# Optimization experiments

Measured on AMD Instinct MI355X. Metric: run time of the kernel, lower is better.

The kernel has to match this reference:

```python
import jax, jax.numpy as jnp
import numpy as np

D_MODEL = 2048
N_HEADS = 16
HEAD_DIM = D_MODEL // N_HEADS  # 128
B, S = 4, 2048


def setup_inputs() -> dict:
    key = jax.random.key(0)
    ks = jax.random.split(key, 7)
    scale = 1.0 / np.sqrt(D_MODEL)
    return {
        "x": jax.random.normal(ks[0], (B, S, D_MODEL), dtype=jnp.float32),
        "cos": jax.random.uniform(ks[1], (S, HEAD_DIM // 2), dtype=jnp.float32),
        "sin": jax.random.uniform(ks[2], (S, HEAD_DIM // 2), dtype=jnp.float32),
        "Wq": jax.random.normal(ks[3], (D_MODEL, D_MODEL), dtype=jnp.float32) * scale,
        "Wk": jax.random.normal(ks[4], (D_MODEL, D_MODEL), dtype=jnp.float32) * scale,
        "Wv": jax.random.normal(ks[5], (D_MODEL, D_MODEL), dtype=jnp.float32) * scale,
        "Wo": jax.random.normal(ks[6], (D_MODEL, D_MODEL), dtype=jnp.float32) * scale,
    }


def apply_rope(x, cos, sin):
    # x: [B, H, S, head_dim]; cos/sin: [S, half] (split-in-half RoPE)
    half = x.shape[-1] // 2
    x1, x2 = x[..., :half], x[..., half:]
    cos = cos[None, None, :, :].astype(x.dtype)
    sin = sin[None, None, :, :].astype(x.dtype)
    return jnp.concatenate([x1 * cos - x2 * sin, x1 * sin + x2 * cos], axis=-1)


def reference(x, cos, sin, Wq, Wk, Wv, Wo):
    Bx, Sx, _ = x.shape
    # nn.Linear: y = x @ W.T
    def proj(W):
        y = jnp.einsum("bsd,ed->bse", x, W)
        return y.reshape(Bx, Sx, N_HEADS, HEAD_DIM).transpose(0, 2, 1, 3)  # [B,H,S,hd]
    q = apply_rope(proj(Wq), cos, sin)
    k = apply_rope(proj(Wk), cos, sin)
    v = proj(Wv)
    scale = 1.0 / np.sqrt(HEAD_DIM)
    scores = jnp.einsum("bhqd,bhkd->bhqk", q, k) * scale  # [B,H,S,S]
    attn = jax.nn.softmax(scores, axis=-1)
    out = jnp.einsum("bhqk,bhkd->bhqd", attn, v)
    out = out.transpose(0, 2, 1, 3).reshape(Bx, Sx, D_MODEL)
    return jnp.einsum("bsd,ed->bse", out, Wo)
```

## Files before the change

### kernel.cpp

```cpp
#include <hip/hip_runtime.h>

typedef _Float16 half_t;
typedef __attribute__((ext_vector_type(8))) _Float16 half8;
typedef __attribute__((ext_vector_type(4))) _Float16 half4v;
typedef __attribute__((ext_vector_type(4))) float f32x4;

#define MFMA16(a,b,c) __builtin_amdgcn_mfma_f32_16x16x32_f16((a),(b),(c),0,0,0)

__device__ __forceinline__ void gld_lds16(const half_t* g, half_t* l){
    __builtin_amdgcn_global_load_lds((__attribute__((address_space(1))) void*)(g),
                                     (__attribute__((address_space(3))) void*)(l), 16, 0, 0);
}

__global__ __launch_bounds__(256) void cvt_k(const float* __restrict__ s, half_t* __restrict__ d, int n4){
    int i = blockIdx.x * 256 + threadIdx.x;
    if (i < n4){
        float4 v = ((const float4*)s)[i];
        half4v h = { (half_t)v.x, (half_t)v.y, (half_t)v.z, (half_t)v.w };
        ((half4v*)d)[i] = h;
    }
}

__global__ __launch_bounds__(256) void cvtw_k(const float* __restrict__ w0, const float* __restrict__ w1,
                                              const float* __restrict__ w2, const float* __restrict__ w3,
                                              half_t* __restrict__ dst){
    const float* srcs[4] = {w0, w1, w2, w3};
    const float* s = srcs[blockIdx.y];
    int i = blockIdx.x * 256 + threadIdx.x;
    float4 v = ((const float4*)s)[i];
    half4v h = { (half_t)v.x, (half_t)v.y, (half_t)v.z, (half_t)v.w };
    ((half4v*)(dst))[(size_t)blockIdx.y * 1048576 + i] = h;
}

__global__ __launch_bounds__(256) void gemm_nt(const half_t* __restrict__ A, const half_t* __restrict__ B,
                                               half_t* __restrict__ Qw, half_t* __restrict__ Kw,
                                               half_t* __restrict__ Vt, float* __restrict__ Co, int kind){
    const int tid  = threadIdx.x;
    const int lane = tid & 63;
    const int w    = lane >> 4;
    const int l15  = lane & 15;
    const int l7   = lane & 7;
    const int wav  = tid >> 6;
    const int wm   = (wav >> 1) * 64;
    const int wn   = (wav & 1) * 64;
    const int bm   = blockIdx.x;
    const int bn   = blockIdx.y;
    const int KD   = 2048;

    __shared__ __align__(16) half_t smem[16384];
    half_t* As = smem;
    half_t* Bs = smem + 8192;

    f32x4 acc[4][4] = {};

    const half_t* Ab = A + (size_t)bm * 128 * KD;
    const half_t* Bb = B + (size_t)bn * 128 * KD;

    for (int k0 = 0; k0 < KD; k0 += 64){
#pragma unroll
        for (int i = 0; i < 4; i++){
            int c = tid + i*256;
            int r = c >> 3, p = c & 7;
            gld_lds16(Ab + (size_t)r*KD + k0 + ((p ^ (r&7)) << 3), As + c*8);
        }
#pragma unroll
        for (int i = 0; i < 4; i++){
            int c = tid + i*256;
            int r = c >> 3, p = c & 7;
            gld_lds16(Bb + (size_t)r*KD + k0 + ((p ^ (r&7)) << 3), Bs + c*8);
        }
        __syncthreads();
#pragma unroll
        for (int ks = 0; ks < 2; ks++){
            half8 af[4], bf[4];
#pragma unroll
            for (int mi = 0; mi < 4; mi++)
                af[mi] = *(const half8*)(As + (wm + mi*16 + l15)*64 + (((ks*4 + w) ^ l7) << 3));
#pragma unroll
            for (int ni = 0; ni < 4; ni++)
                bf[ni] = *(const half8*)(Bs + (wn + ni*16 + l15)*64 + (((ks*4 + w) ^ l7) << 3));
#pragma unroll
            for (int mi = 0; mi < 4; mi++)
#pragma unroll
                for (int ni = 0; ni < 4; ni++)
                    acc[mi][ni] = MFMA16(af[mi], bf[ni], acc[mi][ni]);
        }
        __syncthreads();
    }

    const int rbase = wm + w*4;
    const int cbase = wn + l15;

    if (kind == 0){
        const int which = bn >> 4;
        const int nb = (bn & 15) * 128;
        if (which < 2){
            half_t* dst = which ? Kw : Qw;
#pragma unroll
            for (int mi = 0; mi < 4; mi++)
#pragma unroll
                for (int ni = 0; ni < 4; ni++)
#pragma unroll
                    for (int r = 0; r < 4; r++){
                        int m = bm*128 + rbase + mi*16 + r;
                        int n = nb + cbase + ni*16;
                        dst[(((size_t)(m>>11)*16 + (n>>7))*2048 + (m&2047))*128 + (n&127)] = (half_t)acc[mi][ni][r];
                    }
        } else {
#pragma unroll
            for (int mi = 0; mi < 4; mi++)
#pragma unroll
                for (int ni = 0; ni < 4; ni++){
                    int m0 = bm*128 + rbase + mi*16;
                    int n  = nb + cbase + ni*16;
                    half4v h = {(half_t)acc[mi][ni][0], (half_t)acc[mi][ni][1],
                                (half_t)acc[mi][ni][2], (half_t)acc[mi][ni][3]};
                    *(half4v*)(Vt + (((size_t)(m0>>11)*16 + (n>>7))*128 + (n&127))*2048 + (m0&2047)) = h;
                }
        }
    } else {
#pragma unroll
        for (int mi = 0; mi < 4; mi++)
#pragma unroll
            for (int ni = 0; ni < 4; ni++)
#pragma unroll
                for (int r = 0; r < 4; r++){
                    int m = bm*128 + rbase + mi*16 + r;
                    int n = bn*128 + cbase + ni*16;
                    Co[(size_t)m*2048 + n] = acc[mi][ni][r];
                }
    }
}

__global__ __launch_bounds__(256) void rope_k(half_t* __restrict__ Qw, half_t* __restrict__ Kw,
                                              const float* __restrict__ cs, const float* __restrict__ sn){
    int t  = blockIdx.x * 256 + threadIdx.x;
    int d  = t & 63;
    int s  = (t >> 6) & 2047;
    int bh = t >> 17;
    float c  = cs[s*64 + d];
    float si = sn[s*64 + d];
    size_t base = ((size_t)bh*2048 + s)*128 + d;
    float q1 = (float)Qw[base], q2 = (float)Qw[base+64];
    Qw[base]    = (half_t)(q1*c - q2*si);
    Qw[base+64] = (half_t)(q1*si + q2*c);
    float k1 = (float)Kw[base], k2 = (float)Kw[base+64];
    Kw[base]    = (half_t)(k1*c - k2*si);
    Kw[base+64] = (half_t)(k1*si + k2*c);
}

__global__ __launch_bounds__(256, 3) void attn_k(const half_t* __restrict__ Q, const half_t* __restrict__ K,
                                                 const half_t* __restrict__ Vt, half_t* __restrict__ AO){
    const int tid  = threadIdx.x;
    const int lane = tid & 63;
    const int w    = lane >> 4;
    const int l15  = lane & 15;
    const int l7   = lane & 7;
    const int wav  = tid >> 6;
    const int qt   = blockIdx.x;
    const int bh   = blockIdx.y;

    __shared__ __align__(16) half_t smem[8192 + 8192 + 4*2304];
    half_t* Ks = smem;
    half_t* Vs = smem + 8192;
    half_t* Ps = smem + 16384 + wav*2304;
    half_t* Ob = smem + wav*4096;

    const half_t* Qb = Q + ((size_t)bh*2048 + qt*128 + wav*32)*128;
    half8 aq[2][4];
#pragma unroll
    for (int qi = 0; qi < 2; qi++)
#pragma unroll
        for (int ks = 0; ks < 4; ks++)
            aq[qi][ks] = *(const half8*)(Qb + (qi*16 + l15)*128 + ks*32 + w*8);

    f32x4 oacc[8][2] = {};
    float m_[2] = {-1e30f, -1e30f};
    float l_[2] = {0.0f, 0.0f};

    const float SSC = 0.08838834764831845f * 1.4426950408889634f;

    for (int kt = 0; kt < 32; kt++){
        const half_t* Kb = K  + ((size_t)bh*2048 + kt*64)*128;
        const half_t* Vb = Vt + (size_t)bh*128*2048 + kt*64;
        __syncthreads();
#pragma unroll
        for (int i = 0; i < 4; i++){
            int c = tid + i*256;
            int key = c >> 4, pc = c & 15;
            gld_lds16(Kb + key*128 + ((pc ^ (key&7)) << 3), Ks + c*8);
        }
#pragma unroll
        for (int i = 0; i < 4; i++){
            int c = tid + i*256;
            int d = c >> 3, pc = c & 7;
            gld_lds16(Vb + (size_t)d*2048 + ((pc ^ (d&7)) << 3), Vs + c*8);
        }
        __syncthreads();

        f32x4 sacc[4][2] = {};
#pragma unroll
        for (int ks = 0; ks < 4; ks++){
#pragma unroll
            for (int t = 0; t < 4; t++){
                half8 kf = *(const half8*)(Ks + (t*16 + l15)*128 + (((ks*4 + w) ^ l7) << 3));
                sacc[t][0] = MFMA16(kf, aq[0][ks], sacc[t][0]);
                sacc[t][1] = MFMA16(kf, aq[1][ks], sacc[t][1]);
            }
        }

#pragma unroll
        for (int qi = 0; qi < 2; qi++){
            float mx = sacc[0][qi][0];
#pragma unroll
            for (int t = 0; t < 4; t++)
#pragma unroll
                for (int r = 0; r < 4; r++) mx = fmaxf(mx, sacc[t][qi][r]);
            mx = fmaxf(mx, __shfl_xor(mx, 16));
            mx = fmaxf(mx, __shfl_xor(mx, 32));
            float mn = fmaxf(m_[qi], mx*SSC);
            float alpha = exp2f(m_[qi] - mn);
            m_[qi] = mn;
            float sum = 0.0f;
#pragma unroll
            for (int t = 0; t < 4; t++){
                float p0 = exp2f(sacc[t][qi][0]*SSC - mn);
                float p1 = exp2f(sacc[t][qi][1]*SSC - mn);
                float p2 = exp2f(sacc[t][qi][2]*SSC - mn);
                float p3 = exp2f(sacc[t][qi][3]*SSC - mn);
                sum += (p0 + p1) + (p2 + p3);
                half4v hv = {(half_t)p0, (half_t)p1, (half_t)p2, (half_t)p3};
                *(half4v*)(Ps + (qi*16 + l15)*72 + t*16 + w*4) = hv;
            }
            sum += __shfl_xor(sum, 16);
            sum += __shfl_xor(sum, 32);
            l_[qi] = l_[qi]*alpha + sum;
#pragma unroll
            for (int t = 0; t < 8; t++)
#pragma unroll
                for (int r = 0; r < 4; r++) oacc[t][qi][r] *= alpha;
        }

#pragma unroll
        for (int c2 = 0; c2 < 2; c2++){
            half8 pf0 = *(const half8*)(Ps + l15*72        + c2*32 + w*8);
            half8 pf1 = *(const half8*)(Ps + (16 + l15)*72 + c2*32 + w*8);
#pragma unroll
            for (int t = 0; t < 8; t++){
                half8 vf = *(const half8*)(Vs + (t*16 + l15)*64 + (((c2*4 + w) ^ l7) << 3));
                oacc[t][0] = MFMA16(vf, pf0, oacc[t][0]);
                oacc[t][1] = MFMA16(vf, pf1, oacc[t][1]);
            }
        }
    }

    float inv[2] = {1.0f / l_[0], 1.0f / l_[1]};
    __syncthreads();
#pragma unroll
    for (int t = 0; t < 8; t++)
#pragma unroll
        for (int qi = 0; qi < 2; qi++){
            int q  = qi*16 + l15;
            int c8 = t*2 + (w>>1);
            int pc = c8 ^ l7;
            half4v hv = {(half_t)(oacc[t][qi][0]*inv[qi]), (half_t)(oacc[t][qi][1]*inv[qi]),
                         (half_t)(oacc[t][qi][2]*inv[qi]), (half_t)(oacc[t][qi][3]*inv[qi])};
            *(half4v*)(Ob + q*128 + pc*8 + (w&1)*4) = hv;
        }
    const int b = bh >> 4, h = bh & 15;
#pragma unroll
    for (int it = 0; it < 8; it++){
        int q  = it*4 + w;
        half8 rd = *(const half8*)(Ob + q*128 + ((l15 ^ (q&7)) << 3));
        int s = qt*128 + wav*32 + q;
        *(half8*)(AO + ((size_t)(b*2048 + s))*2048 + h*128 + l15*8) = rd;
    }
}

extern "C" void kernel_launch(void* const* d_in, const int* in_sizes, int n_in,
                              void* d_out, int out_size, void* d_ws, size_t ws_size,
                              hipStream_t stream){
    const float* x  = (const float*)d_in[0];
    const float* cs = (const float*)d_in[1];
    const float* sn = (const float*)d_in[2];
    const float* Wq = (const float*)d_in[3];
    const float* Wk = (const float*)d_in[4];
    const float* Wv = (const float*)d_in[5];
    const float* Wo = (const float*)d_in[6];

    half_t* ws = (half_t*)d_ws;
    half_t* xh = ws;
    half_t* w4 = ws + (size_t)16777216;
    half_t* qw = ws + (size_t)33554432;
    half_t* kw = ws + (size_t)50331648;
    half_t* vt = ws + (size_t)67108864;
    half_t* ao = ws + (size_t)83886080;

    cvt_k<<<16384, 256, 0, stream>>>(x, xh, 4194304);
    cvtw_k<<<dim3(4096, 4), 256, 0, stream>>>(Wq, Wk, Wv, Wo, w4);

    gemm_nt<<<dim3(64, 48), 256, 0, stream>>>(xh, w4, qw, kw, vt, nullptr, 0);
    rope_k<<<32768, 256, 0, stream>>>(qw, kw, cs, sn);
    attn_k<<<dim3(16, 64), 256, 0, stream>>>(qw, kw, vt, ao);
    gemm_nt<<<dim3(64, 16), 256, 0, stream>>>(ao, w4 + 12582912, nullptr, nullptr, nullptr,
                                              (float*)d_out, 1);
}
```

Baseline: 786.7 us.

## Split attention over two key halves and merge partial outputs

Measured after the change: 833.6 us. +6.0%, slower.

```diff
diff --git a/kernel.cpp b/kernel.cpp
--- a/kernel.cpp
+++ b/kernel.cpp
@@ -150,14 +150,16 @@
 }
 
 __global__ __launch_bounds__(256, 3) void attn_k(const half_t* __restrict__ Q, const half_t* __restrict__ K,
-                                                 const half_t* __restrict__ Vt, half_t* __restrict__ AO){
+                                                 const half_t* __restrict__ Vt, half_t* __restrict__ PO0,
+                                                 half_t* __restrict__ PO1, float* __restrict__ ML){
     const int tid  = threadIdx.x;
     const int lane = tid & 63;
     const int w    = lane >> 4;
     const int l15  = lane & 15;
     const int l7   = lane & 7;
     const int wav  = tid >> 6;
-    const int qt   = blockIdx.x;
+    const int qt   = blockIdx.x & 15;
+    const int kh   = blockIdx.x >> 4;
     const int bh   = blockIdx.y;
 
     __shared__ __align__(16) half_t smem[8192 + 8192 + 4*2304];
@@ -180,7 +182,8 @@
 
     const float SSC = 0.08838834764831845f * 1.4426950408889634f;
 
-    for (int kt = 0; kt < 32; kt++){
+    const int kt0 = kh << 4;
+    for (int kt = kt0; kt < kt0 + 16; kt++){
         const half_t* Kb = K  + ((size_t)bh*2048 + kt*64)*128;
         const half_t* Vb = Vt + (size_t)bh*128*2048 + kt*64;
         __syncthreads();
@@ -218,27 +221,33 @@
                 for (int r = 0; r < 4; r++) mx = fmaxf(mx, sacc[t][qi][r]);
             mx = fmaxf(mx, __shfl_xor(mx, 16));
             mx = fmaxf(mx, __shfl_xor(mx, 32));
-            float mn = fmaxf(m_[qi], mx*SSC);
-            float alpha = exp2f(m_[qi] - mn);
-            m_[qi] = mn;
+            float mxs = mx * SSC;
+            unsigned long long upd = __ballot(mxs > m_[qi]);
+            if (upd){
+                float mn    = fmaxf(m_[qi], mxs);
+                float alpha = exp2f(m_[qi] - mn);
+                m_[qi] = mn;
+                l_[qi] *= alpha;
+#pragma unroll
+                for (int t = 0; t < 8; t++)
+#pragma unroll
+                    for (int r = 0; r < 4; r++) oacc[t][qi][r] *= alpha;
+            }
+            float mq = m_[qi];
             float sum = 0.0f;
 #pragma unroll
             for (int t = 0; t < 4; t++){
-                float p0 = exp2f(sacc[t][qi][0]*SSC - mn);
-                float p1 = exp2f(sacc[t][qi][1]*SSC - mn);
-                float p2 = exp2f(sacc[t][qi][2]*SSC - mn);
-                float p3 = exp2f(sacc[t][qi][3]*SSC - mn);
+                float p0 = exp2f(sacc[t][qi][0]*SSC - mq);
+                float p1 = exp2f(sacc[t][qi][1]*SSC - mq);
+                float p2 = exp2f(sacc[t][qi][2]*SSC - mq);
+                float p3 = exp2f(sacc[t][qi][3]*SSC - mq);
                 sum += (p0 + p1) + (p2 + p3);
                 half4v hv = {(half_t)p0, (half_t)p1, (half_t)p2, (half_t)p3};
                 *(half4v*)(Ps + (qi*16 + l15)*72 + t*16 + w*4) = hv;
             }
             sum += __shfl_xor(sum, 16);
             sum += __shfl_xor(sum, 32);
-            l_[qi] = l_[qi]*alpha + sum;
-#pragma unroll
-            for (int t = 0; t < 8; t++)
-#pragma unroll
-                for (int r = 0; r < 4; r++) oacc[t][qi][r] *= alpha;
+            l_[qi] += sum;
         }
 
 #pragma unroll
@@ -254,7 +263,17 @@
         }
     }
 
+    if (w == 0){
+#pragma unroll
+        for (int qi = 0; qi < 2; qi++){
+            int srow = bh*2048 + qt*128 + wav*32 + qi*16 + l15;
+            ML[(size_t)(kh*2)*131072     + srow] = m_[qi];
+            ML[(size_t)(kh*2 + 1)*131072 + srow] = l_[qi];
+        }
+    }
+
     float inv[2] = {1.0f / l_[0], 1.0f / l_[1]};
+    half_t* DST = kh ? PO1 : PO0;
     __syncthreads();
 #pragma unroll
     for (int t = 0; t < 8; t++)
@@ -273,8 +292,34 @@
         int q  = it*4 + w;
         half8 rd = *(const half8*)(Ob + q*128 + ((l15 ^ (q&7)) << 3));
         int s = qt*128 + wav*32 + q;
-        *(half8*)(AO + ((size_t)(b*2048 + s))*2048 + h*128 + l15*8) = rd;
-    }
+        *(half8*)(DST + ((size_t)(b*2048 + s))*2048 + h*128 + l15*8) = rd;
+    }
+}
+
+__global__ __launch_bounds__(256) void merge_k(const half_t* __restrict__ P0, const half_t* __restrict__ P1,
+                                               const float* __restrict__ ML, half_t* __restrict__ AO){
+    int t   = blockIdx.x * 256 + threadIdx.x;
+    int row = t >> 4;
+    int c   = t & 15;
+    float m1 = ML[row];
+    float l1 = ML[131072 + row];
+    float m2 = ML[262144 + row];
+    float l2 = ML[393216 + row];
+    float M  = fmaxf(m1, m2);
+    float w1 = exp2f(m1 - M) * l1;
+    float w2 = exp2f(m2 - M) * l2;
+    float inv = 1.0f / (w1 + w2);
+    float a1 = w1 * inv, a2 = w2 * inv;
+    int bh = row >> 11, s = row & 2047;
+    int b = bh >> 4, h = bh & 15;
+    size_t idx = ((size_t)(b*2048 + s))*2048 + h*128 + c*8;
+    half8 x1 = *(const half8*)(P0 + idx);
+    half8 x2 = *(const half8*)(P1 + idx);
+    half8 o;
+#pragma unroll
+    for (int j = 0; j < 8; j++)
+        o[j] = (half_t)(a1*(float)x1[j] + a2*(float)x2[j]);
+    *(half8*)(AO + idx) = o;
 }
 
 extern "C" void kernel_launch(void* const* d_in, const int* in_sizes, int n_in,
@@ -296,12 +341,17 @@
     half_t* vt = ws + (size_t)67108864;
     half_t* ao = ws + (size_t)83886080;
 
+    half_t* p0 = xh;
+    half_t* p1 = (half_t*)d_out;
+    float*  ml = (float*)((char*)d_out + 33554432);
+
     cvt_k<<<16384, 256, 0, stream>>>(x, xh, 4194304);
     cvtw_k<<<dim3(4096, 4), 256, 0, stream>>>(Wq, Wk, Wv, Wo, w4);
 
     gemm_nt<<<dim3(64, 48), 256, 0, stream>>>(xh, w4, qw, kw, vt, nullptr, 0);
     rope_k<<<32768, 256, 0, stream>>>(qw, kw, cs, sn);
-    attn_k<<<dim3(16, 64), 256, 0, stream>>>(qw, kw, vt, ao);
+    attn_k<<<dim3(32, 64), 256, 0, stream>>>(qw, kw, vt, p0, p1, ml);
+    merge_k<<<8192, 256, 0, stream>>>(p0, p1, ml, ao);
     gemm_nt<<<dim3(64, 16), 256, 0, stream>>>(ao, w4 + 12582912, nullptr, nullptr, nullptr,
                                               (float*)d_out, 1);
 }
```
